# Kernel optimization log

Measured on AMD Instinct MI355X. Metric: run time of the kernel, lower is better.

Reference implementation:

```python
import jax, jax.numpy as jnp
import numpy as np

D = 1024
SCALE = 10.0  # forward does qk.div(1/10) == qk * 10


def setup_inputs() -> dict:
    key = jax.random.key(0)
    ks = jax.random.split(key, 9)
    B, S = 8, 2048
    lim = 1.0 / np.sqrt(D)  # torch Linear default init range
    return {
        "query": jax.random.normal(ks[0], (B, S, D), jnp.float32),
        "key": jax.random.normal(ks[1], (B, S, D), jnp.float32),
        "value": jax.random.normal(ks[2], (B, S, D), jnp.float32),
        "Wq": jax.random.uniform(ks[3], (D, D), jnp.float32, -lim, lim),
        "bq": jax.random.uniform(ks[4], (D,), jnp.float32, -lim, lim),
        "Wk": jax.random.uniform(ks[5], (D, D), jnp.float32, -lim, lim),
        "bk": jax.random.uniform(ks[6], (D,), jnp.float32, -lim, lim),
        "Wv": jax.random.uniform(ks[7], (D, D), jnp.float32, -lim, lim),
        "bv": jax.random.uniform(ks[8], (D,), jnp.float32, -lim, lim),
    }


def reference(query, key, value, Wq, bq, Wk, bk, Wv, bv):
    # torch Linear: x @ W.T + b
    q = jnp.einsum("bsd,ed->bse", query, Wq) + bq
    k = jnp.einsum("bsd,ed->bse", key, Wk) + bk
    v = jnp.einsum("bsd,ed->bse", value, Wv) + bv
    qk = jnp.einsum("bqd,bkd->bqk", q, k)
    scaled_qk = qk * SCALE  # qk.div(1.0 / scale_factor)
    softmax_qk = jax.nn.softmax(scaled_qk, axis=-1)
    # dropout in eval mode == identity (deterministic reference)
    output = jnp.einsum("bqk,bkd->bqd", softmax_qk, v)
    return (output, softmax_qk)
```

## Files before the change

kernel.cpp:

```cpp
#include <hip/hip_runtime.h>

typedef unsigned short u16;
typedef unsigned int u32;
typedef __bf16 bf16x8 __attribute__((ext_vector_type(8)));
typedef float f32x4 __attribute__((ext_vector_type(4)));

__device__ __forceinline__ u16 bf16_rne(float f) {
  u32 u = __float_as_uint(f);
  u += 0x7fffu + ((u >> 16) & 1u);
  return (u16)(u >> 16);
}
__device__ __forceinline__ float bf16_to_f(u16 h) {
  return __uint_as_float(((u32)h) << 16);
}
__device__ __forceinline__ void gload16(const u16* g, u16* l) {
  __builtin_amdgcn_global_load_lds(
      (const __attribute__((address_space(1))) void*)g,
      (__attribute__((address_space(3))) void*)l, 16, 0, 0);
}

__global__ __launch_bounds__(256) void split_kernel(const float* __restrict__ x,
                                                    u16* __restrict__ hi,
                                                    u16* __restrict__ lo, int n8) {
  int i = blockIdx.x * 256 + threadIdx.x;
  if (i >= n8) return;
  float4 a = ((const float4*)x)[2 * i];
  float4 b = ((const float4*)x)[2 * i + 1];
  float v[8] = {a.x, a.y, a.z, a.w, b.x, b.y, b.z, b.w};
  union { u16 u[8]; uint4 q; } H, L;
#pragma unroll
  for (int j = 0; j < 8; ++j) H.u[j] = bf16_rne(v[j]);
  ((uint4*)hi)[i] = H.q;
  if (lo != nullptr) {
#pragma unroll
    for (int j = 0; j < 8; ++j) L.u[j] = bf16_rne(v[j] - bf16_to_f(H.u[j]));
    ((uint4*)lo)[i] = L.q;
  }
}

__global__ __launch_bounds__(256) void transpose_split(const float* __restrict__ in,
                                                       u16* __restrict__ hiT,
                                                       u16* __restrict__ loT) {
  __shared__ float tile[32][33];
  const int t = threadIdx.x;
  const int r0 = blockIdx.y * 32, c0 = blockIdx.x * 32;
  const int x = t & 31, y = t >> 5;
#pragma unroll
  for (int i = 0; i < 4; ++i)
    tile[y + i * 8][x] = in[(size_t)(r0 + y + i * 8) * 1024 + c0 + x];
  __syncthreads();
#pragma unroll
  for (int i = 0; i < 4; ++i) {
    float v = tile[x][y + i * 8];
    u16 h = bf16_rne(v);
    u16 l = bf16_rne(v - bf16_to_f(h));
    size_t o = (size_t)(c0 + y + i * 8) * 1024 + r0 + x;
    hiT[o] = h;
    loT[o] = l;
  }
}

__global__ __launch_bounds__(256) void zero_vec(float* __restrict__ h) {
  h[blockIdx.x * 256 + threadIdx.x] = 0.f;
}

__global__ __launch_bounds__(256) void colvec_kernel(const float* __restrict__ W,
                                                     const float* __restrict__ b,
                                                     float* __restrict__ h) {
  __shared__ float sb[16];
  const int t = threadIdx.x;
  const int e0 = blockIdx.x * 16;
  if (t < 16) sb[t] = b[e0 + t];
  __syncthreads();
  float a0 = 0.f, a1 = 0.f, a2 = 0.f, a3 = 0.f;
#pragma unroll
  for (int i = 0; i < 16; ++i) {
    const float* row = W + (size_t)(e0 + i) * 1024;
    const float be = sb[i];
    a0 += row[t] * be;
    a1 += row[t + 256] * be;
    a2 += row[t + 512] * be;
    a3 += row[t + 768] * be;
  }
  atomicAdd(&h[t], a0);
  atomicAdd(&h[t + 256], a1);
  atomicAdd(&h[t + 512], a2);
  atomicAdd(&h[t + 768], a3);
}

__global__ __launch_bounds__(256) void rowdot_kernel(const float* __restrict__ X,
                                                     const float* __restrict__ h,
                                                     float* __restrict__ w) {
  const int t = threadIdx.x, lane = t & 63, wv = t >> 6;
  const size_t row = (size_t)blockIdx.x * 4 + wv;
  const float4* xr = (const float4*)(X + row * 1024);
  const float4* hr = (const float4*)h;
  float acc = 0.f;
#pragma unroll
  for (int j = 0; j < 4; ++j) {
    float4 a = xr[lane + j * 64];
    float4 b = hr[lane + j * 64];
    acc += a.x * b.x + a.y * b.y + a.z * b.z + a.w * b.w;
  }
#pragma unroll
  for (int o = 32; o > 0; o >>= 1) acc += __shfl_xor(acc, o, 64);
  if (lane == 0) w[row] = acc;
}

template <int NPROD, int EPI>
__global__ __launch_bounds__(256) void gemm_bt(
    const u16* __restrict__ Ah, const u16* __restrict__ Al,
    const u16* __restrict__ Bh, const u16* __restrict__ Bl,
    const float* __restrict__ bias,
    u16* __restrict__ Ch, u16* __restrict__ Cl,
    float* __restrict__ Cf, float scale, int K,
    int lda, int ldb, int ldc,
    long long batchA, long long batchB, long long batchC) {
  __shared__ u16 sAh[4096];
  __shared__ u16 sBh[4096];
  __shared__ u16 sAl[NPROD == 3 ? 4096 : 64];
  __shared__ u16 sBl[NPROD == 3 ? 4096 : 64];

  const int t = threadIdx.x;
  const int w = t >> 6;
  const int lane = t & 63;
  const int m0 = blockIdx.y * 128;
  const int n0 = blockIdx.x * 128;
  const long long z = blockIdx.z;

  Ah += z * batchA;
  Bh += z * batchB;

  const int rS = t >> 2;
  const int cS = (((t & 3) ^ ((t >> 3) & 3))) * 8;
  const u16* pAh = Ah + (size_t)(m0 + rS) * lda + cS;
  const u16* pBh = Bh + (size_t)(n0 + rS) * ldb + cS;
  const u16* pAl = nullptr;
  const u16* pBl = nullptr;
  if constexpr (NPROD == 3) {
    pAl = Al + z * batchA + (size_t)(m0 + rS) * lda + cS;
    pBl = Bl + z * batchB + (size_t)(n0 + rS) * ldb + cS;
  }

  const int wr = (w >> 1) * 64;
  const int wc = (w & 1) * 64;
  const int fr = lane & 15;
  const int cc = lane >> 4;
  const int fk = (cc ^ ((fr >> 1) & 3)) * 8;

  f32x4 acc[4][4];
#pragma unroll
  for (int i = 0; i < 4; ++i)
#pragma unroll
    for (int j = 0; j < 4; ++j) acc[i][j] = (f32x4){0.f, 0.f, 0.f, 0.f};

  for (int k0 = 0; k0 < K; k0 += 32) {
    __syncthreads();
#pragma unroll
    for (int j = 0; j < 2; ++j) {
      gload16(pAh + (size_t)j * 64 * lda + k0, &sAh[j * 2048 + w * 512]);
      gload16(pBh + (size_t)j * 64 * ldb + k0, &sBh[j * 2048 + w * 512]);
      if constexpr (NPROD == 3) {
        gload16(pAl + (size_t)j * 64 * lda + k0, &sAl[j * 2048 + w * 512]);
        gload16(pBl + (size_t)j * 64 * ldb + k0, &sBl[j * 2048 + w * 512]);
      }
    }
    __syncthreads();
    bf16x8 ah[4], bh[4], al[4], bl[4];
#pragma unroll
    for (int i = 0; i < 4; ++i) {
      ah[i] = *(const bf16x8*)&sAh[(wr + i * 16 + fr) * 32 + fk];
      bh[i] = *(const bf16x8*)&sBh[(wc + i * 16 + fr) * 32 + fk];
      if constexpr (NPROD == 3) {
        al[i] = *(const bf16x8*)&sAl[(wr + i * 16 + fr) * 32 + fk];
        bl[i] = *(const bf16x8*)&sBl[(wc + i * 16 + fr) * 32 + fk];
      }
    }
#pragma unroll
    for (int i = 0; i < 4; ++i)
#pragma unroll
      for (int j = 0; j < 4; ++j) {
        acc[i][j] = __builtin_amdgcn_mfma_f32_16x16x32_bf16(ah[i], bh[j], acc[i][j], 0, 0, 0);
        if constexpr (NPROD == 3) {
          acc[i][j] = __builtin_amdgcn_mfma_f32_16x16x32_bf16(ah[i], bl[j], acc[i][j], 0, 0, 0);
          acc[i][j] = __builtin_amdgcn_mfma_f32_16x16x32_bf16(al[i], bh[j], acc[i][j], 0, 0, 0);
        }
      }
  }

  if constexpr (EPI >= 2) Cf += z * batchC;

#pragma unroll
  for (int i = 0; i < 4; ++i) {
    const int row0 = m0 + wr + i * 16 + ((lane >> 4) << 2);
#pragma unroll
    for (int j = 0; j < 4; ++j) {
      const int col = n0 + wc + j * 16 + (lane & 15);
      if constexpr (EPI == 0) {
        const float b = bias ? bias[col] : 0.0f;
#pragma unroll
        for (int r = 0; r < 4; ++r) {
          float c = acc[i][j][r] + b;
          u16 h = bf16_rne(c);
          u16 l = bf16_rne(c - bf16_to_f(h));
          size_t o = (size_t)(row0 + r) * ldc + col;
          Ch[o] = h;
          Cl[o] = l;
        }
      } else if constexpr (EPI == 1) {
        const float b = bias[col];
        ushort4 pk;
        pk.x = bf16_rne(acc[i][j][0] + b);
        pk.y = bf16_rne(acc[i][j][1] + b);
        pk.z = bf16_rne(acc[i][j][2] + b);
        pk.w = bf16_rne(acc[i][j][3] + b);
        const int bb = row0 >> 11;
        const int s = row0 & 2047;
        *(ushort4*)&Ch[(size_t)bb * 2097152 + (size_t)col * 2048 + s] = pk;
      } else if constexpr (EPI == 2) {
#pragma unroll
        for (int r = 0; r < 4; ++r)
          Cf[(size_t)(row0 + r) * ldc + col] = acc[i][j][r] * scale;
      } else {
        const float wv = bias[(size_t)z * 2048 + col];
#pragma unroll
        for (int r = 0; r < 4; ++r)
          Cf[(size_t)(row0 + r) * ldc + col] = (acc[i][j][r] + wv) * scale;
      }
    }
  }
}

template <int NPROD, int EPI>
__global__ __launch_bounds__(512) void gemm256(
    const u16* __restrict__ Ah, const u16* __restrict__ Al,
    const u16* __restrict__ Bh, const u16* __restrict__ Bl,
    const float* __restrict__ bias,
    u16* __restrict__ Ch, u16* __restrict__ Cl,
    float* __restrict__ Cf, float scale, int K,
    int lda, int ldb, int ldc,
    long long batchA, long long batchB, long long batchC) {
  __shared__ u16 sAh[2][8192];
  __shared__ u16 sBh[2][8192];
  __shared__ u16 sAl[NPROD == 3 ? 16384 : 8];
  __shared__ u16 sBl[NPROD == 3 ? 16384 : 8];

  const int t = threadIdx.x;
  const int w = t >> 6;
  const int lane = t & 63;

  const u32 gx = gridDim.x;
  const u32 gxy = gridDim.x * gridDim.y;
  const u32 total = gxy * gridDim.z;
  const u32 h = blockIdx.x + gridDim.x * (blockIdx.y + gridDim.y * blockIdx.z);
  const u32 l = (h & 7) * (total >> 3) + (h >> 3);
  const u32 bz = l / gxy;
  const u32 rem = l - bz * gxy;
  const u32 by = rem / gx;
  const u32 bx = rem - by * gx;
  const int m0 = by * 256;
  const int n0 = bx * 256;
  const long long z = bz;

  const int rS = t >> 2;
  const int cS = ((t & 3) ^ ((rS >> 1) & 3)) * 8;
  const u16* pAh = Ah + z * batchA + (size_t)(m0 + rS) * lda + cS;
  const u16* pBh = Bh + z * batchB + (size_t)(n0 + rS) * ldb + cS;
  const u16* pAl = nullptr;
  const u16* pBl = nullptr;
  if constexpr (NPROD == 3) {
    pAl = Al + z * batchA + (size_t)(m0 + rS) * lda + cS;
    pBl = Bl + z * batchB + (size_t)(n0 + rS) * ldb + cS;
  }

  const int wr = (w >> 2) * 128;
  const int wc = (w & 3) * 64;
  const int fr = lane & 15;
  const int fk = (((lane >> 4) ^ ((fr >> 1) & 3)) * 8);

  f32x4 acc[8][4];
#pragma unroll
  for (int i = 0; i < 8; ++i)
#pragma unroll
    for (int j = 0; j < 4; ++j) acc[i][j] = (f32x4){0.f, 0.f, 0.f, 0.f};

  auto SAH = [&](int b, int k0) {
    gload16(pAh + k0, &sAh[b][w * 512]);
    gload16(pAh + (size_t)128 * lda + k0, &sAh[b][4096 + w * 512]);
  };
  auto SBH = [&](int b, int k0) {
    gload16(pBh + k0, &sBh[b][w * 512]);
    gload16(pBh + (size_t)128 * ldb + k0, &sBh[b][4096 + w * 512]);
  };
  auto SAL = [&](int b, int k0) {
    gload16(pAl + k0, &sAl[b * 8192 + w * 512]);
    gload16(pAl + (size_t)128 * lda + k0, &sAl[b * 8192 + 4096 + w * 512]);
  };
  auto SBL = [&](int b, int k0) {
    gload16(pBl + k0, &sBl[b * 8192 + w * 512]);
    gload16(pBl + (size_t)128 * ldb + k0, &sBl[b * 8192 + 4096 + w * 512]);
  };

  SAH(0, 0);
  SBH(0, 0);
  if constexpr (NPROD == 3) {
    SAL(0, 0);
    SBL(0, 0);
  }
  asm volatile("s_waitcnt vmcnt(0)" ::: "memory");
  asm volatile("s_barrier" ::: "memory");

  const int nt = K >> 5;
  for (int kt = 0; kt < nt; ++kt) {
    const int cur = kt & 1;
    const int nxt = cur ^ 1;

    if (kt + 1 < nt) {
      const int kn = (kt + 1) << 5;
      SAH(nxt, kn);
      SBH(nxt, kn);
      if constexpr (NPROD == 3) {
        SAL(nxt, kn);
        SBL(nxt, kn);
      }
    }

    if constexpr (NPROD == 3) {
      bf16x8 bh[4], bl[4];
#pragma unroll
      for (int n = 0; n < 4; ++n) {
        bh[n] = *(const bf16x8*)&sBh[cur][(wc + n * 16 + fr) * 32 + fk];
        bl[n] = *(const bf16x8*)&sBl[cur * 8192 + (wc + n * 16 + fr) * 32 + fk];
      }
#pragma unroll
      for (int q = 0; q < 4; ++q) {
        bf16x8 a0h = *(const bf16x8*)&sAh[cur][(wr + (2 * q) * 16 + fr) * 32 + fk];
        bf16x8 a1h = *(const bf16x8*)&sAh[cur][(wr + (2 * q + 1) * 16 + fr) * 32 + fk];
        bf16x8 a0l = *(const bf16x8*)&sAl[cur * 8192 + (wr + (2 * q) * 16 + fr) * 32 + fk];
        bf16x8 a1l = *(const bf16x8*)&sAl[cur * 8192 + (wr + (2 * q + 1) * 16 + fr) * 32 + fk];
        __builtin_amdgcn_s_setprio(1);
#pragma unroll
        for (int n = 0; n < 4; ++n) {
          acc[2 * q][n] = __builtin_amdgcn_mfma_f32_16x16x32_bf16(a0h, bh[n], acc[2 * q][n], 0, 0, 0);
          acc[2 * q + 1][n] = __builtin_amdgcn_mfma_f32_16x16x32_bf16(a1h, bh[n], acc[2 * q + 1][n], 0, 0, 0);
        }
#pragma unroll
        for (int n = 0; n < 4; ++n) {
          acc[2 * q][n] = __builtin_amdgcn_mfma_f32_16x16x32_bf16(a0h, bl[n], acc[2 * q][n], 0, 0, 0);
          acc[2 * q + 1][n] = __builtin_amdgcn_mfma_f32_16x16x32_bf16(a1h, bl[n], acc[2 * q + 1][n], 0, 0, 0);
        }
#pragma unroll
        for (int n = 0; n < 4; ++n) {
          acc[2 * q][n] = __builtin_amdgcn_mfma_f32_16x16x32_bf16(a0l, bh[n], acc[2 * q][n], 0, 0, 0);
          acc[2 * q + 1][n] = __builtin_amdgcn_mfma_f32_16x16x32_bf16(a1l, bh[n], acc[2 * q + 1][n], 0, 0, 0);
        }
        __builtin_amdgcn_s_setprio(0);
      }
    } else {
      bf16x8 bh[4];
#pragma unroll
      for (int n = 0; n < 4; ++n)
        bh[n] = *(const bf16x8*)&sBh[cur][(wc + n * 16 + fr) * 32 + fk];
#pragma unroll
      for (int q = 0; q < 2; ++q) {
        bf16x8 af[4];
#pragma unroll
        for (int i = 0; i < 4; ++i)
          af[i] = *(const bf16x8*)&sAh[cur][(wr + (4 * q + i) * 16 + fr) * 32 + fk];
        __builtin_amdgcn_s_setprio(1);
#pragma unroll
        for (int i = 0; i < 4; ++i)
#pragma unroll
          for (int n = 0; n < 4; ++n)
            acc[4 * q + i][n] = __builtin_amdgcn_mfma_f32_16x16x32_bf16(af[i], bh[n], acc[4 * q + i][n], 0, 0, 0);
        __builtin_amdgcn_s_setprio(0);
      }
    }

    asm volatile("s_waitcnt vmcnt(0)" ::: "memory");
    asm volatile("s_barrier" ::: "memory");
  }

  if constexpr (EPI >= 2) Cf += z * batchC;

#pragma unroll
  for (int i = 0; i < 8; ++i) {
    const int row0 = m0 + wr + i * 16 + ((lane >> 4) << 2);
#pragma unroll
    for (int j = 0; j < 4; ++j) {
      const int col = n0 + wc + j * 16 + (lane & 15);
      if constexpr (EPI == 0) {
        const float bsv = bias ? bias[col] : 0.0f;
#pragma unroll
        for (int r = 0; r < 4; ++r) {
          float c = acc[i][j][r] + bsv;
          u16 h = bf16_rne(c);
          u16 l = bf16_rne(c - bf16_to_f(h));
          size_t o = (size_t)(row0 + r) * ldc + col;
          Ch[o] = h;
          Cl[o] = l;
        }
      } else if constexpr (EPI == 1) {
        const float bsv = bias[col];
        ushort4 pk;
        pk.x = bf16_rne(acc[i][j][0] + bsv);
        pk.y = bf16_rne(acc[i][j][1] + bsv);
        pk.z = bf16_rne(acc[i][j][2] + bsv);
        pk.w = bf16_rne(acc[i][j][3] + bsv);
        const int bb = row0 >> 11;
        const int s = row0 & 2047;
        *(ushort4*)&Ch[(size_t)bb * 2097152 + (size_t)col * 2048 + s] = pk;
      } else if constexpr (EPI == 2) {
#pragma unroll
        for (int r = 0; r < 4; ++r)
          Cf[(size_t)(row0 + r) * ldc + col] = acc[i][j][r] * scale;
      } else {
        const float wv = bias[(size_t)z * 2048 + col];
#pragma unroll
        for (int r = 0; r < 4; ++r)
          Cf[(size_t)(row0 + r) * ldc + col] = (acc[i][j][r] + wv) * scale;
      }
    }
  }
}

__global__ __launch_bounds__(256) void softmax_kernel(float* __restrict__ L,
                                                      u16* __restrict__ P) {
  const size_t row = blockIdx.x;
  float* r = L + row * 2048;
  u16* p = P + row * 2048;
  const int t = threadIdx.x;
  const int w = t >> 6;
  const int lane = t & 63;

  float4 v0 = ((const float4*)r)[2 * t];
  float4 v1 = ((const float4*)r)[2 * t + 1];
  float e[8] = {v0.x, v0.y, v0.z, v0.w, v1.x, v1.y, v1.z, v1.w};

  float vm = e[0];
#pragma unroll
  for (int j = 1; j < 8; ++j) vm = fmaxf(vm, e[j]);
#pragma unroll
  for (int o = 32; o > 0; o >>= 1) vm = fmaxf(vm, __shfl_xor(vm, o, 64));
  __shared__ float redm[4], reds[4];
  if (lane == 0) redm[w] = vm;
  __syncthreads();
  vm = fmaxf(fmaxf(redm[0], redm[1]), fmaxf(redm[2], redm[3]));

  float s = 0.f;
#pragma unroll
  for (int j = 0; j < 8; ++j) {
    e[j] = __expf(e[j] - vm);
    s += e[j];
  }
#pragma unroll
  for (int o = 32; o > 0; o >>= 1) s += __shfl_xor(s, o, 64);
  if (lane == 0) reds[w] = s;
  __syncthreads();
  s = reds[0] + reds[1] + reds[2] + reds[3];
  const float inv = 1.0f / s;

  float4 o0, o1;
  o0.x = e[0] * inv; o0.y = e[1] * inv; o0.z = e[2] * inv; o0.w = e[3] * inv;
  o1.x = e[4] * inv; o1.y = e[5] * inv; o1.z = e[6] * inv; o1.w = e[7] * inv;
  ((float4*)r)[2 * t] = o0;
  ((float4*)r)[2 * t + 1] = o1;
  union { u16 u[8]; uint4 q; } pk;
  pk.u[0] = bf16_rne(o0.x); pk.u[1] = bf16_rne(o0.y);
  pk.u[2] = bf16_rne(o0.z); pk.u[3] = bf16_rne(o0.w);
  pk.u[4] = bf16_rne(o1.x); pk.u[5] = bf16_rne(o1.y);
  pk.u[6] = bf16_rne(o1.z); pk.u[7] = bf16_rne(o1.w);
  ((uint4*)p)[t] = pk.q;
}

extern "C" void kernel_launch(void* const* d_in, const int* in_sizes, int n_in,
                              void* d_out, int out_size, void* d_ws, size_t ws_size,
                              hipStream_t stream) {
  const float* Xq = (const float*)d_in[0];
  const float* Xk = (const float*)d_in[1];
  const float* Xv = (const float*)d_in[2];
  const float* Wq = (const float*)d_in[3];
  const float* bq = (const float*)d_in[4];
  const float* Wk = (const float*)d_in[5];
  const float* bk = (const float*)d_in[6];
  const float* Wv = (const float*)d_in[7];
  const float* bv = (const float*)d_in[8];
  (void)bk;

  char* out = (char*)d_out;
  char* ws = (char*)d_ws;

  u16* T_hi = (u16*)(out + 0);
  u16* T_lo = (u16*)(out + 33554432);
  u16* Xq_hi = (u16*)(out + 67108864);
  u16* Xq_lo = (u16*)(out + 100663296);
  u16* Xv_hi = (u16*)(out + 134217728);
  u16* Mt_hi = (u16*)(out + 167772160);
  u16* Mt_lo = (u16*)(out + 171966464);
  float* logits = (float*)(out + 67108864);
  float* outO = (float*)(out + 0);

  u16* WqT_hi = (u16*)(ws + 0);
  u16* WqT_lo = (u16*)(ws + 2097152);
  u16* WkT_hi = (u16*)(ws + 4194304);
  u16* WkT_lo = (u16*)(ws + 6291456);
  u16* Wv_hi = (u16*)(ws + 8388608);
  u16* P = (u16*)(ws + 0);
  float* hvec = (float*)(ws + 67108864);
  float* wvec = (float*)(ws + 67112960);
  u16* Xk_hi = (u16*)(ws + 67178496);
  u16* Xk_lo = (u16*)(ws + 100732928);
  u16* Vt = (u16*)(ws + 134287360);

  transpose_split<<<dim3(32, 32), 256, 0, stream>>>(Wq, WqT_hi, WqT_lo);
  transpose_split<<<dim3(32, 32), 256, 0, stream>>>(Wk, WkT_hi, WkT_lo);
  zero_vec<<<4, 256, 0, stream>>>(hvec);
  colvec_kernel<<<64, 256, 0, stream>>>(Wk, bq, hvec);
  split_kernel<<<512, 256, 0, stream>>>(Wv, Wv_hi, nullptr, 131072);

  split_kernel<<<8192, 256, 0, stream>>>(Xk, Xk_hi, Xk_lo, 2097152);
  rowdot_kernel<<<4096, 256, 0, stream>>>(Xk, hvec, wvec);
  split_kernel<<<8192, 256, 0, stream>>>(Xq, Xq_hi, Xq_lo, 2097152);
  split_kernel<<<8192, 256, 0, stream>>>(Xv, Xv_hi, nullptr, 2097152);

  gemm_bt<3, 0><<<dim3(8, 8, 1), 256, 0, stream>>>(
      WkT_hi, WkT_lo, WqT_hi, WqT_lo, nullptr, Mt_hi, Mt_lo, nullptr, 1.f,
      1024, 1024, 1024, 1024, 0, 0, 0);
  gemm256<1, 1><<<dim3(4, 64, 1), 512, 0, stream>>>(
      Xv_hi, nullptr, Wv_hi, nullptr, bv, Vt, nullptr, nullptr, 1.f,
      1024, 1024, 1024, 1024, 0, 0, 0);
  gemm256<3, 0><<<dim3(4, 64, 1), 512, 0, stream>>>(
      Xq_hi, Xq_lo, Mt_hi, Mt_lo, nullptr, T_hi, T_lo, nullptr, 1.f,
      1024, 1024, 1024, 1024, 0, 0, 0);
  gemm256<3, 3><<<dim3(8, 8, 8), 512, 0, stream>>>(
      T_hi, T_lo, Xk_hi, Xk_lo, wvec, nullptr, nullptr, logits, 10.f,
      1024, 1024, 1024, 2048, 2048LL * 1024, 2048LL * 1024, 2048LL * 2048);
  softmax_kernel<<<16384, 256, 0, stream>>>(logits, P);
  gemm256<1, 2><<<dim3(4, 8, 8), 512, 0, stream>>>(
      P, nullptr, Vt, nullptr, nullptr, nullptr, nullptr, outO, 1.f,
      2048, 2048, 2048, 1024, 2048LL * 2048, 1024LL * 2048, 2048LL * 1024);
}
```

Baseline: 911.8 us.

## Pipeline GEMM main loop with partial vmcnt waits and LDS fragment prefetch

Moves the global-to-LDS wait to the top of each k-iteration, using partial vmcnt counts so only the current buffer's loads must be complete while the next tile's loads stay in flight. The A-fragment LDS reads are software-pipelined one step ahead of the MFMA groups, with explicit lgkmcnt waits and sched_barriers to fix the instruction order. The aim is to hide LDS read latency behind MFMAs and to cut stall time at barriers. It costs extra VGPRs for the fragment buffers, which could lower occupancy, and it depends on the hand-counted waitcnt values being correct.

After: 898.3 us. No clear change (-1.5%).

```diff
diff --git a/kernel.cpp b/kernel.cpp
--- a/kernel.cpp
+++ b/kernel.cpp
@@ -307,15 +307,14 @@
     SAL(0, 0);
     SBL(0, 0);
   }
-  asm volatile("s_waitcnt vmcnt(0)" ::: "memory");
-  asm volatile("s_barrier" ::: "memory");
 
   const int nt = K >> 5;
   for (int kt = 0; kt < nt; ++kt) {
     const int cur = kt & 1;
     const int nxt = cur ^ 1;
-
-    if (kt + 1 < nt) {
+    const bool pf = (kt + 1) < nt;
+
+    if (pf) {
       const int kn = (kt + 1) << 5;
       SAH(nxt, kn);
       SBH(nxt, kn);
@@ -324,60 +323,95 @@
         SBL(nxt, kn);
       }
     }
+    __builtin_amdgcn_sched_barrier(0);
+    if (pf) {
+      if constexpr (NPROD == 3)
+        asm volatile("s_waitcnt vmcnt(8)" ::: "memory");
+      else
+        asm volatile("s_waitcnt vmcnt(4)" ::: "memory");
+    } else {
+      asm volatile("s_waitcnt vmcnt(0)" ::: "memory");
+    }
+    __builtin_amdgcn_sched_barrier(0);
+    asm volatile("s_barrier" ::: "memory");
 
     if constexpr (NPROD == 3) {
-      bf16x8 bh[4], bl[4];
+      bf16x8 bh[4], bl[4], a[4][4];
 #pragma unroll
       for (int n = 0; n < 4; ++n) {
         bh[n] = *(const bf16x8*)&sBh[cur][(wc + n * 16 + fr) * 32 + fk];
         bl[n] = *(const bf16x8*)&sBl[cur * 8192 + (wc + n * 16 + fr) * 32 + fk];
       }
+      a[0][0] = *(const bf16x8*)&sAh[cur][(wr + 0 * 16 + fr) * 32 + fk];
+      a[0][1] = *(const bf16x8*)&sAh[cur][(wr + 1 * 16 + fr) * 32 + fk];
+      a[0][2] = *(const bf16x8*)&sAl[cur * 8192 + (wr + 0 * 16 + fr) * 32 + fk];
+      a[0][3] = *(const bf16x8*)&sAl[cur * 8192 + (wr + 1 * 16 + fr) * 32 + fk];
 #pragma unroll
       for (int q = 0; q < 4; ++q) {
-        bf16x8 a0h = *(const bf16x8*)&sAh[cur][(wr + (2 * q) * 16 + fr) * 32 + fk];
-        bf16x8 a1h = *(const bf16x8*)&sAh[cur][(wr + (2 * q + 1) * 16 + fr) * 32 + fk];
-        bf16x8 a0l = *(const bf16x8*)&sAl[cur * 8192 + (wr + (2 * q) * 16 + fr) * 32 + fk];
-        bf16x8 a1l = *(const bf16x8*)&sAl[cur * 8192 + (wr + (2 * q + 1) * 16 + fr) * 32 + fk];
+        if (q < 3) {
+          a[q + 1][0] = *(const bf16x8*)&sAh[cur][(wr + (2 * q + 2) * 16 + fr) * 32 + fk];
+          a[q + 1][1] = *(const bf16x8*)&sAh[cur][(wr + (2 * q + 3) * 16 + fr) * 32 + fk];
+          a[q + 1][2] = *(const bf16x8*)&sAl[cur * 8192 + (wr + (2 * q + 2) * 16 + fr) * 32 + fk];
+          a[q + 1][3] = *(const bf16x8*)&sAl[cur * 8192 + (wr + (2 * q + 3) * 16 + fr) * 32 + fk];
+        }
+        __builtin_amdgcn_sched_barrier(0);
+        if (q < 3)
+          asm volatile("s_waitcnt lgkmcnt(4)" ::: "memory");
+        else
+          asm volatile("s_waitcnt lgkmcnt(0)" ::: "memory");
+        __builtin_amdgcn_sched_barrier(0);
         __builtin_amdgcn_s_setprio(1);
 #pragma unroll
         for (int n = 0; n < 4; ++n) {
-          acc[2 * q][n] = __builtin_amdgcn_mfma_f32_16x16x32_bf16(a0h, bh[n], acc[2 * q][n], 0, 0, 0);
-          acc[2 * q + 1][n] = __builtin_amdgcn_mfma_f32_16x16x32_bf16(a1h, bh[n], acc[2 * q + 1][n], 0, 0, 0);
+          acc[2 * q][n] = __builtin_amdgcn_mfma_f32_16x16x32_bf16(a[q][0], bh[n], acc[2 * q][n], 0, 0, 0);
+          acc[2 * q + 1][n] = __builtin_amdgcn_mfma_f32_16x16x32_bf16(a[q][1], bh[n], acc[2 * q + 1][n], 0, 0, 0);
         }
 #pragma unroll
         for (int n = 0; n < 4; ++n) {
-          acc[2 * q][n] = __builtin_amdgcn_mfma_f32_16x16x32_bf16(a0h, bl[n], acc[2 * q][n], 0, 0, 0);
-          acc[2 * q + 1][n] = __builtin_amdgcn_mfma_f32_16x16x32_bf16(a1h, bl[n], acc[2 * q + 1][n], 0, 0, 0);
+          acc[2 * q][n] = __builtin_amdgcn_mfma_f32_16x16x32_bf16(a[q][0], bl[n], acc[2 * q][n], 0, 0, 0);
+          acc[2 * q + 1][n] = __builtin_amdgcn_mfma_f32_16x16x32_bf16(a[q][1], bl[n], acc[2 * q + 1][n], 0, 0, 0);
         }
 #pragma unroll
         for (int n = 0; n < 4; ++n) {
-          acc[2 * q][n] = __builtin_amdgcn_mfma_f32_16x16x32_bf16(a0l, bh[n], acc[2 * q][n], 0, 0, 0);
-          acc[2 * q + 1][n] = __builtin_amdgcn_mfma_f32_16x16x32_bf16(a1l, bh[n], acc[2 * q + 1][n], 0, 0, 0);
+          acc[2 * q][n] = __builtin_amdgcn_mfma_f32_16x16x32_bf16(a[q][2], bh[n], acc[2 * q][n], 0, 0, 0);
+          acc[2 * q + 1][n] = __builtin_amdgcn_mfma_f32_16x16x32_bf16(a[q][3], bh[n], acc[2 * q + 1][n], 0, 0, 0);
         }
         __builtin_amdgcn_s_setprio(0);
+        __builtin_amdgcn_sched_barrier(0);
       }
     } else {
-      bf16x8 bh[4];
+      bf16x8 bh[4], a[2][4];
 #pragma unroll
       for (int n = 0; n < 4; ++n)
         bh[n] = *(const bf16x8*)&sBh[cur][(wc + n * 16 + fr) * 32 + fk];
 #pragma unroll
+      for (int i = 0; i < 4; ++i)
+        a[0][i] = *(const bf16x8*)&sAh[cur][(wr + i * 16 + fr) * 32 + fk];
+#pragma unroll
       for (int q = 0; q < 2; ++q) {
-        bf16x8 af[4];
+        if (q < 1) {
+#pragma unroll
+          for (int i = 0; i < 4; ++i)
+            a[1][i] = *(const bf16x8*)&sAh[cur][(wr + (4 + i) * 16 + fr) * 32 + fk];
+        }
+        __builtin_amdgcn_sched_barrier(0);
+        if (q < 1)
+          asm volatile("s_waitcnt lgkmcnt(4)" ::: "memory");
+        else
+          asm volatile("s_waitcnt lgkmcnt(0)" ::: "memory");
+        __builtin_amdgcn_sched_barrier(0);
+        __builtin_amdgcn_s_setprio(1);
 #pragma unroll
         for (int i = 0; i < 4; ++i)
-          af[i] = *(const bf16x8*)&sAh[cur][(wr + (4 * q + i) * 16 + fr) * 32 + fk];
-        __builtin_amdgcn_s_setprio(1);
-#pragma unroll
-        for (int i = 0; i < 4; ++i)
 #pragma unroll
           for (int n = 0; n < 4; ++n)
-            acc[4 * q + i][n] = __builtin_amdgcn_mfma_f32_16x16x32_bf16(af[i], bh[n], acc[4 * q + i][n], 0, 0, 0);
+            acc[4 * q + i][n] = __builtin_amdgcn_mfma_f32_16x16x32_bf16(a[q][i], bh[n], acc[4 * q + i][n], 0, 0, 0);
         __builtin_amdgcn_s_setprio(0);
-      }
-    }
-
-    asm volatile("s_waitcnt vmcnt(0)" ::: "memory");
+        __builtin_amdgcn_sched_barrier(0);
+      }
+    }
+
+    asm volatile("s_waitcnt lgkmcnt(0)" ::: "memory");
     asm volatile("s_barrier" ::: "memory");
   }
 
```

## Interleave next-tile global-to-LDS loads with MFMA phases using fine-grained barriers

Applied to the files above, without the earlier changes.

Restructures the GEMM main loop so prefetch of the next K tile is split across compute phases: A-hi is issued before the wait, and the B-hi, A-lo and B-lo loads are issued between MFMA sub-blocks. Partial vmcnt waits and extra s_barriers with sched_barrier fences replace the single full drain at the end of each iteration. The aim is to overlap global-to-LDS traffic with matrix math and keep waves in lockstep, in the style of ping-pong scheduling. The added barriers per iteration bring more synchronization overhead, and the correctness of the vmcnt(2) accounting relies on the exact issue order of the loads.

Result: no change. 900.8 us (-1.2%).

```diff
diff --git a/kernel.cpp b/kernel.cpp
--- a/kernel.cpp
+++ b/kernel.cpp
@@ -307,37 +307,70 @@
     SAL(0, 0);
     SBL(0, 0);
   }
-  asm volatile("s_waitcnt vmcnt(0)" ::: "memory");
-  asm volatile("s_barrier" ::: "memory");
 
   const int nt = K >> 5;
   for (int kt = 0; kt < nt; ++kt) {
     const int cur = kt & 1;
     const int nxt = cur ^ 1;
-
-    if (kt + 1 < nt) {
-      const int kn = (kt + 1) << 5;
-      SAH(nxt, kn);
-      SBH(nxt, kn);
-      if constexpr (NPROD == 3) {
-        SAL(nxt, kn);
-        SBL(nxt, kn);
-      }
-    }
+    const bool pf = (kt + 1) < nt;
+    const int kn = (kt + 1) << 5;
 
     if constexpr (NPROD == 3) {
       bf16x8 bh[4], bl[4];
+      bf16x8 a0h, a1h, a0l, a1l;
+      if (pf) SAH(nxt, kn);
+      __builtin_amdgcn_sched_barrier(0);
+      if (pf)
+        asm volatile("s_waitcnt vmcnt(2)" ::: "memory");
+      else
+        asm volatile("s_waitcnt vmcnt(0)" ::: "memory");
+      __builtin_amdgcn_sched_barrier(0);
+      asm volatile("s_barrier" ::: "memory");
 #pragma unroll
       for (int n = 0; n < 4; ++n) {
         bh[n] = *(const bf16x8*)&sBh[cur][(wc + n * 16 + fr) * 32 + fk];
         bl[n] = *(const bf16x8*)&sBl[cur * 8192 + (wc + n * 16 + fr) * 32 + fk];
       }
-#pragma unroll
-      for (int q = 0; q < 4; ++q) {
-        bf16x8 a0h = *(const bf16x8*)&sAh[cur][(wr + (2 * q) * 16 + fr) * 32 + fk];
-        bf16x8 a1h = *(const bf16x8*)&sAh[cur][(wr + (2 * q + 1) * 16 + fr) * 32 + fk];
-        bf16x8 a0l = *(const bf16x8*)&sAl[cur * 8192 + (wr + (2 * q) * 16 + fr) * 32 + fk];
-        bf16x8 a1l = *(const bf16x8*)&sAl[cur * 8192 + (wr + (2 * q + 1) * 16 + fr) * 32 + fk];
+      a0h = *(const bf16x8*)&sAh[cur][(wr + 0 * 16 + fr) * 32 + fk];
+      a1h = *(const bf16x8*)&sAh[cur][(wr + 1 * 16 + fr) * 32 + fk];
+      a0l = *(const bf16x8*)&sAl[cur * 8192 + (wr + 0 * 16 + fr) * 32 + fk];
+      a1l = *(const bf16x8*)&sAl[cur * 8192 + (wr + 1 * 16 + fr) * 32 + fk];
+      asm volatile("s_waitcnt lgkmcnt(0)" ::: "memory");
+      __builtin_amdgcn_sched_barrier(0);
+      __builtin_amdgcn_s_setprio(1);
+#pragma unroll
+      for (int n = 0; n < 4; ++n) {
+        acc[0][n] = __builtin_amdgcn_mfma_f32_16x16x32_bf16(a0h, bh[n], acc[0][n], 0, 0, 0);
+        acc[1][n] = __builtin_amdgcn_mfma_f32_16x16x32_bf16(a1h, bh[n], acc[1][n], 0, 0, 0);
+      }
+#pragma unroll
+      for (int n = 0; n < 4; ++n) {
+        acc[0][n] = __builtin_amdgcn_mfma_f32_16x16x32_bf16(a0h, bl[n], acc[0][n], 0, 0, 0);
+        acc[1][n] = __builtin_amdgcn_mfma_f32_16x16x32_bf16(a1h, bl[n], acc[1][n], 0, 0, 0);
+      }
+#pragma unroll
+      for (int n = 0; n < 4; ++n) {
+        acc[0][n] = __builtin_amdgcn_mfma_f32_16x16x32_bf16(a0l, bh[n], acc[0][n], 0, 0, 0);
+        acc[1][n] = __builtin_amdgcn_mfma_f32_16x16x32_bf16(a1l, bh[n], acc[1][n], 0, 0, 0);
+      }
+      __builtin_amdgcn_s_setprio(0);
+      __builtin_amdgcn_sched_barrier(0);
+      asm volatile("s_barrier" ::: "memory");
+#pragma unroll
+      for (int q = 1; q < 4; ++q) {
+        if (pf) {
+          if (q == 1) SBH(nxt, kn);
+          if (q == 2) SAL(nxt, kn);
+          if (q == 3) SBL(nxt, kn);
+        }
+        a0h = *(const bf16x8*)&sAh[cur][(wr + (2 * q) * 16 + fr) * 32 + fk];
+        a1h = *(const bf16x8*)&sAh[cur][(wr + (2 * q + 1) * 16 + fr) * 32 + fk];
+        a0l = *(const bf16x8*)&sAl[cur * 8192 + (wr + (2 * q) * 16 + fr) * 32 + fk];
+        a1l = *(const bf16x8*)&sAl[cur * 8192 + (wr + (2 * q + 1) * 16 + fr) * 32 + fk];
+        __builtin_amdgcn_sched_barrier(0);
+        asm volatile("s_barrier" ::: "memory");
+        asm volatile("s_waitcnt lgkmcnt(0)" ::: "memory");
+        __builtin_amdgcn_sched_barrier(0);
         __builtin_amdgcn_s_setprio(1);
 #pragma unroll
         for (int n = 0; n < 4; ++n) {
@@ -355,30 +388,54 @@
           acc[2 * q + 1][n] = __builtin_amdgcn_mfma_f32_16x16x32_bf16(a1l, bh[n], acc[2 * q + 1][n], 0, 0, 0);
         }
         __builtin_amdgcn_s_setprio(0);
+        __builtin_amdgcn_sched_barrier(0);
+        asm volatile("s_barrier" ::: "memory");
       }
     } else {
-      bf16x8 bh[4];
+      bf16x8 bh[4], af[4];
+      if (pf) SAH(nxt, kn);
+      __builtin_amdgcn_sched_barrier(0);
+      if (pf)
+        asm volatile("s_waitcnt vmcnt(2)" ::: "memory");
+      else
+        asm volatile("s_waitcnt vmcnt(0)" ::: "memory");
+      __builtin_amdgcn_sched_barrier(0);
+      asm volatile("s_barrier" ::: "memory");
 #pragma unroll
       for (int n = 0; n < 4; ++n)
         bh[n] = *(const bf16x8*)&sBh[cur][(wc + n * 16 + fr) * 32 + fk];
 #pragma unroll
-      for (int q = 0; q < 2; ++q) {
-        bf16x8 af[4];
-#pragma unroll
-        for (int i = 0; i < 4; ++i)
-          af[i] = *(const bf16x8*)&sAh[cur][(wr + (4 * q + i) * 16 + fr) * 32 + fk];
-        __builtin_amdgcn_s_setprio(1);
-#pragma unroll
-        for (int i = 0; i < 4; ++i)
-#pragma unroll
-          for (int n = 0; n < 4; ++n)
-            acc[4 * q + i][n] = __builtin_amdgcn_mfma_f32_16x16x32_bf16(af[i], bh[n], acc[4 * q + i][n], 0, 0, 0);
-        __builtin_amdgcn_s_setprio(0);
-      }
+      for (int i = 0; i < 4; ++i)
+        af[i] = *(const bf16x8*)&sAh[cur][(wr + i * 16 + fr) * 32 + fk];
+      asm volatile("s_waitcnt lgkmcnt(0)" ::: "memory");
+      __builtin_amdgcn_sched_barrier(0);
+      __builtin_amdgcn_s_setprio(1);
+#pragma unroll
+      for (int i = 0; i < 4; ++i)
+#pragma unroll
+        for (int n = 0; n < 4; ++n)
+          acc[i][n] = __builtin_amdgcn_mfma_f32_16x16x32_bf16(af[i], bh[n], acc[i][n], 0, 0, 0);
+      __builtin_amdgcn_s_setprio(0);
+      __builtin_amdgcn_sched_barrier(0);
+      asm volatile("s_barrier" ::: "memory");
+      if (pf) SBH(nxt, kn);
+#pragma unroll
+      for (int i = 0; i < 4; ++i)
+        af[i] = *(const bf16x8*)&sAh[cur][(wr + (4 + i) * 16 + fr) * 32 + fk];
+      __builtin_amdgcn_sched_barrier(0);
+      asm volatile("s_barrier" ::: "memory");
+      asm volatile("s_waitcnt lgkmcnt(0)" ::: "memory");
+      __builtin_amdgcn_sched_barrier(0);
+      __builtin_amdgcn_s_setprio(1);
+#pragma unroll
+      for (int i = 0; i < 4; ++i)
+#pragma unroll
+        for (int n = 0; n < 4; ++n)
+          acc[4 + i][n] = __builtin_amdgcn_mfma_f32_16x16x32_bf16(af[i], bh[n], acc[4 + i][n], 0, 0, 0);
+      __builtin_amdgcn_s_setprio(0);
+      __builtin_amdgcn_sched_barrier(0);
+      asm volatile("s_barrier" ::: "memory");
     }
-
-    asm volatile("s_waitcnt vmcnt(0)" ::: "memory");
-    asm volatile("s_barrier" ::: "memory");
   }
 
   if constexpr (EPI >= 2) Cf += z * batchC;
```
